# Performance work log

Measured on AMD Instinct MI355X. Metric: run time of the kernel, lower is better.

Reference implementation:

```python
import jax, jax.numpy as jnp
import numpy as np

B, C, N, H = 16, 256, 2048, 128


def setup_inputs() -> dict:
    key = jax.random.key(0)
    ks = jax.random.split(key, 9)
    s_in = 1.0 / np.sqrt(C)
    s_h = 1.0 / np.sqrt(H)
    return {
        "x": jax.random.normal(ks[0], (B, C, N), dtype=jnp.float32),
        "Wq": jax.random.uniform(ks[1], (H, C), jnp.float32, -s_in, s_in),
        "bq": jax.random.uniform(ks[2], (H,), jnp.float32, -s_in, s_in),
        "Wk": jax.random.uniform(ks[3], (H, C), jnp.float32, -s_in, s_in),
        "bk": jax.random.uniform(ks[4], (H,), jnp.float32, -s_in, s_in),
        "Wv": jax.random.uniform(ks[5], (H, C), jnp.float32, -s_in, s_in),
        "bv": jax.random.uniform(ks[6], (H,), jnp.float32, -s_in, s_in),
        "Wf": jax.random.uniform(ks[7], (C, H), jnp.float32, -s_h, s_h),
        "bf": jax.random.uniform(ks[8], (C,), jnp.float32, -s_h, s_h),
    }


def reference(x, Wq, bq, Wk, bk, Wv, bv, Wf, bf):
    # 1x1 conv == channel-wise linear: [B,C,N] -> [B,H,N]
    Q = jnp.einsum("bcn,hc->bhn", x, Wq) + bq[:, None]
    K = jnp.einsum("bcn,hc->bhn", x, Wk) + bk[:, None]
    V = jnp.einsum("bcn,hc->bhn", x, Wv) + bv[:, None]
    # attn[b, i, j] = softmax_j( Q[b,:,i] . K[b,:,j] )   (no sqrt(d) scaling, as in source)
    scores = jnp.einsum("bhi,bhj->bij", Q, K)          # [B, N, N]
    attn = jax.nn.softmax(scores, axis=-1)
    # out[b, h, i] = sum_j V[b,h,j] * attn[b,i,j]
    out = jnp.einsum("bhj,bij->bhi", V, attn)           # [B, H, N]
    out = jnp.einsum("bhn,ch->bcn", out, Wf) + bf[:, None]
    return out + x
```

## Files before the change

### kernel.cpp

```cpp
#include <hip/hip_runtime.h>
#include <hip/hip_bf16.h>

#define BATCH 16
#define CDIM 256
#define NDIM 2048
#define HDIM 128
#define KVB 128
#define NT (NDIM / KVB)

typedef __bf16 bf16;
typedef float f32x4 __attribute__((ext_vector_type(4)));
typedef float f32x16 __attribute__((ext_vector_type(16)));
typedef bf16 bf16x8 __attribute__((ext_vector_type(8)));
typedef unsigned int u32x4 __attribute__((ext_vector_type(4)));

#define LOG2E 1.4426950408889634f

__device__ __forceinline__ int swz512(int row, int colbyte) {
  return row * 512 + (colbyte ^ ((row & 15) << 4));
}
__device__ __forceinline__ int swz256(int row, int colbyte) {
  return row * 256 + (colbyte ^ ((row & 7) << 4));
}

__device__ __forceinline__ f32x4 mfma16(bf16x8 a, bf16x8 b, f32x4 c) {
  return __builtin_amdgcn_mfma_f32_16x16x32_bf16(a, b, c, 0, 0, 0);
}
__device__ __forceinline__ f32x16 mfma32(bf16x8 a, bf16x8 b, f32x16 c) {
  return __builtin_amdgcn_mfma_f32_32x32x16_bf16(a, b, c, 0, 0, 0);
}

__device__ __forceinline__ unsigned cvtpk(float lo, float hi) {
  unsigned r;
  asm("v_cvt_pk_bf16_f32 %0, %1, %2" : "=v"(r) : "v"(lo), "v"(hi));
  return r;
}
__device__ __forceinline__ void pswap(unsigned &a, unsigned &b) {
  asm volatile("v_permlane32_swap_b32 %0, %1" : "+v"(a), "+v"(b));
}

__device__ __forceinline__ void gload16(const bf16* g, char* l) {
  __builtin_amdgcn_global_load_lds(
      (const __attribute__((address_space(1))) void*)g,
      (__attribute__((address_space(3))) void*)l, 16, 0, 0);
}

__device__ __forceinline__ bf16x8 cvt8(float4 a, float4 b) {
  bf16x8 o;
  o[0] = (bf16)a.x; o[1] = (bf16)a.y; o[2] = (bf16)a.z; o[3] = (bf16)a.w;
  o[4] = (bf16)b.x; o[5] = (bf16)b.y; o[6] = (bf16)b.z; o[7] = (bf16)b.w;
  return o;
}

__global__ __launch_bounds__(256) void k1_qkv(
    const float* __restrict__ x,
    const float* __restrict__ Wq, const float* __restrict__ bq,
    const float* __restrict__ Wk, const float* __restrict__ bk,
    const float* __restrict__ Wv, const float* __restrict__ bv,
    bf16* __restrict__ Qo, bf16* __restrict__ Ko, bf16* __restrict__ Vo) {
  __shared__ char lds[65536];
  char* xT = lds;
  char* Wt = lds + 32768;

  const int t = threadIdx.x;
  const int l = t & 63;
  const int w = t >> 6;
  const int b = blockIdx.x >> 5;
  const int n0 = (blockIdx.x & 31) * 64;

#pragma unroll
  for (int pass = 0; pass < 16; ++pass) {
    int c = pass * 16 + (t >> 4);
    int nq = t & 15;
    const float4 v = *reinterpret_cast<const float4*>(
        x + (size_t)(b * CDIM + c) * NDIM + n0 + nq * 4);
    float fv[4] = {v.x, v.y, v.z, v.w};
#pragma unroll
    for (int i = 0; i < 4; ++i) {
      int row = nq * 4 + i;
      *reinterpret_cast<bf16*>(xT + swz512(row, c * 2)) = (bf16)fv[i];
    }
  }

  const float* Wp[3] = {Wq, Wk, Wv};
  const float* bp[3] = {bq, bk, bv};

#pragma unroll 1
  for (int p = 0; p < 3; ++p) {
    f32x4 acc[8];
#pragma unroll
    for (int i = 0; i < 8; ++i) acc[i] = f32x4{0.f, 0.f, 0.f, 0.f};

#pragma unroll 1
    for (int kh = 0; kh < 2; ++kh) {
      __syncthreads();
#pragma unroll
      for (int pass = 0; pass < 8; ++pass) {
        int h = pass * 16 + (t >> 4);
        int cq = t & 15;
        const float* src = Wp[p] + (size_t)h * CDIM + kh * 128 + cq * 8;
        float4 v0 = *reinterpret_cast<const float4*>(src);
        float4 v1 = *reinterpret_cast<const float4*>(src + 4);
        *reinterpret_cast<bf16x8*>(Wt + swz256(h, cq * 16)) = cvt8(v0, v1);
      }
      __syncthreads();

      if (p < 2) {
#pragma unroll
        for (int ks = 0; ks < 4; ++ks) {
          int cb2 = ks * 64 + (l >> 4) * 16;
          bf16x8 a = *reinterpret_cast<const bf16x8*>(
              xT + swz512(w * 16 + (l & 15), kh * 256 + cb2));
#pragma unroll
          for (int nf = 0; nf < 8; ++nf) {
            bf16x8 bb = *reinterpret_cast<const bf16x8*>(
                Wt + swz256(nf * 16 + (l & 15), cb2));
            acc[nf] = mfma16(a, bb, acc[nf]);
          }
        }
      } else {
#pragma unroll
        for (int ks = 0; ks < 4; ++ks) {
          int cb2 = ks * 64 + (l >> 4) * 16;
          bf16x8 a0 = *reinterpret_cast<const bf16x8*>(
              Wt + swz256(w * 32 + (l & 15), cb2));
          bf16x8 a1 = *reinterpret_cast<const bf16x8*>(
              Wt + swz256(w * 32 + 16 + (l & 15), cb2));
#pragma unroll
          for (int nf = 0; nf < 4; ++nf) {
            bf16x8 bb = *reinterpret_cast<const bf16x8*>(
                xT + swz512(nf * 16 + (l & 15), kh * 256 + cb2));
            acc[nf] = mfma16(a0, bb, acc[nf]);
            acc[4 + nf] = mfma16(a1, bb, acc[4 + nf]);
          }
        }
      }
    }

    if (p < 2) {
      bf16* dst = (p == 0) ? Qo : Ko;
#pragma unroll
      for (int nf = 0; nf < 8; ++nf) {
        float bias = bp[p][nf * 16 + (l & 15)];
#pragma unroll
        for (int r = 0; r < 4; ++r) {
          int n = n0 + w * 16 + (l >> 4) * 4 + r;
          int h = nf * 16 + (l & 15);
          dst[(size_t)(b * NDIM + n) * HDIM + h] = (bf16)(acc[nf][r] + bias);
        }
      }
    } else {
#pragma unroll
      for (int mf = 0; mf < 2; ++mf)
#pragma unroll
        for (int nf = 0; nf < 4; ++nf)
#pragma unroll
          for (int r = 0; r < 4; ++r) {
            int h = w * 32 + mf * 16 + (l >> 4) * 4 + r;
            int n = n0 + nf * 16 + (l & 15);
            Vo[(size_t)(b * HDIM + h) * NDIM + n] =
                (bf16)(acc[mf * 4 + nf][r] + bp[2][h]);
          }
    }
  }
}

__global__ __launch_bounds__(512, 2) void k2_attn(
    const bf16* __restrict__ Q, const bf16* __restrict__ K,
    const bf16* __restrict__ V, bf16* __restrict__ O) {
  extern __shared__ char lds[];

  const int t = threadIdx.x;
  const int l = t & 63;
  const int w = t >> 6;
  const int wm = w >> 1;
  const int wk = w & 1;
  const int hi = l >> 5;
  const int c31 = l & 31;

  const int pid = blockIdx.x;
  const int b = (pid & 7) * 2 + ((pid >> 3) >> 4);
  const int q0 = ((pid >> 3) & 15) * 128;

  bf16x8 qf[8];
  {
    const bf16* qrow = Q + (size_t)(b * NDIM + q0 + wm * 32 + c31) * HDIM + hi * 8;
#pragma unroll
    for (int cs = 0; cs < 8; ++cs)
      qf[cs] = *reinterpret_cast<const bf16x8*>(qrow + cs * 16);
  }

  const bool isV = (w >= 4);
  const int wv = isV ? (w - 4) : w;
  const int slot = l & 15;
  const bf16* gbase[8];
#pragma unroll
  for (int i = 0; i < 8; ++i) {
    int r = wv * 32 + (l >> 4) + i * 4;
    int so = (slot ^ (r & 15)) * 8;
    gbase[i] = isV ? (V + (size_t)(b * HDIM + r) * NDIM + so)
                   : (K + (size_t)(b * NDIM + r) * HDIM + so);
  }
  const size_t gstep = isV ? (size_t)KVB : (size_t)KVB * HDIM;
  const int stagebase = (isV ? 32768 : 0) + wv * 8192;

  f32x16 oacc[4];
#pragma unroll
  for (int dg = 0; dg < 4; ++dg)
#pragma unroll
    for (int r = 0; r < 16; ++r) oacc[dg][r] = 0.f;
  float m_run = -1.0e30f, l_run = 0.f;

#pragma unroll
  for (int i = 0; i < 8; ++i)
    gload16(gbase[i], lds + stagebase + i * 1024);

#pragma unroll 1
  for (int kt = 0; kt < NT; ++kt) {
    char* buf = lds + (kt & 1) * 65536;
    if (kt + 1 < NT) {
      char* nbuf = lds + ((kt + 1) & 1) * 65536;
      const size_t off = (size_t)(kt + 1) * gstep;
#pragma unroll
      for (int i = 0; i < 8; ++i)
        gload16(gbase[i] + off, nbuf + stagebase + i * 1024);
      asm volatile("s_waitcnt vmcnt(8)" ::: "memory");
    } else {
      asm volatile("s_waitcnt vmcnt(0)" ::: "memory");
    }
    __builtin_amdgcn_s_barrier();

    const char* Kt = buf;
    const char* Vt = buf + 32768;
    const int rx = l & 15;

    f32x16 s[2];
#pragma unroll
    for (int kg = 0; kg < 2; ++kg)
#pragma unroll
      for (int r = 0; r < 16; ++r) s[kg][r] = 0.f;
    __builtin_amdgcn_s_setprio(1);
#pragma unroll
    for (int kg = 0; kg < 2; ++kg) {
      const char* kr = Kt + (wk * 64 + kg * 32 + c31) * 256;
#pragma unroll
      for (int cs = 0; cs < 8; ++cs) {
        bf16x8 kf = *reinterpret_cast<const bf16x8*>(kr + (((cs * 2 + hi) ^ rx) * 16));
        s[kg] = mfma32(kf, qf[cs], s[kg]);
      }
    }
    __builtin_amdgcn_s_setprio(0);

    float mt = s[0][0];
#pragma unroll
    for (int r = 1; r < 16; ++r) mt = fmaxf(mt, s[0][r]);
#pragma unroll
    for (int r = 0; r < 16; ++r) mt = fmaxf(mt, s[1][r]);
    mt = fmaxf(mt, __shfl_xor(mt, 32));

    float fac = 1.0f;
    if (!__all(mt - m_run <= 8.0f)) {
      float mnew = fmaxf(m_run, mt);
      fac = __builtin_amdgcn_exp2f((m_run - mnew) * LOG2E);
      m_run = mnew;
      int fbits = __builtin_bit_cast(int, fac);
#pragma unroll
      for (int r = 0; r < 16; ++r) {
        int srcl = ((r & 3) + 8 * (r >> 2) + 4 * hi) * 4;
        float fr = __builtin_bit_cast(
            float, __builtin_amdgcn_ds_bpermute(srcl, fbits));
#pragma unroll
        for (int dg = 0; dg < 4; ++dg) oacc[dg][r] *= fr;
      }
    }

    float sum = 0.f;
#pragma unroll
    for (int kg = 0; kg < 2; ++kg)
#pragma unroll
      for (int r = 0; r < 16; ++r) {
        float p = __builtin_amdgcn_exp2f((s[kg][r] - m_run) * LOG2E);
        s[kg][r] = p;
        sum += p;
      }
    sum += __shfl_xor(sum, 32);
    l_run = l_run * fac + sum;

    __builtin_amdgcn_s_setprio(1);
#pragma unroll
    for (int kg = 0; kg < 2; ++kg) {
      unsigned w0 = cvtpk(s[kg][0], s[kg][1]);
      unsigned w1 = cvtpk(s[kg][2], s[kg][3]);
      unsigned w2 = cvtpk(s[kg][4], s[kg][5]);
      unsigned w3 = cvtpk(s[kg][6], s[kg][7]);
      unsigned w4 = cvtpk(s[kg][8], s[kg][9]);
      unsigned w5 = cvtpk(s[kg][10], s[kg][11]);
      unsigned w6 = cvtpk(s[kg][12], s[kg][13]);
      unsigned w7 = cvtpk(s[kg][14], s[kg][15]);
      pswap(w0, w2); pswap(w1, w3); pswap(w4, w6); pswap(w5, w7);
      u32x4 pw0 = {w0, w1, w2, w3};
      u32x4 pw1 = {w4, w5, w6, w7};
      bf16x8 pa0 = __builtin_bit_cast(bf16x8, pw0);
      bf16x8 pa1 = __builtin_bit_cast(bf16x8, pw1);
#pragma unroll
      for (int dg = 0; dg < 4; ++dg) {
        const char* vr = Vt + (dg * 32 + c31) * 256;
        bf16x8 vf0 = *reinterpret_cast<const bf16x8*>(
            vr + (((wk * 8 + kg * 4 + 0 + hi) ^ rx) * 16));
        oacc[dg] = mfma32(pa0, vf0, oacc[dg]);
        bf16x8 vf1 = *reinterpret_cast<const bf16x8*>(
            vr + (((wk * 8 + kg * 4 + 2 + hi) ^ rx) * 16));
        oacc[dg] = mfma32(pa1, vf1, oacc[dg]);
      }
    }
    __builtin_amdgcn_s_setprio(0);
    __builtin_amdgcn_s_barrier();
  }

  float* O1 = (float*)lds;
  float* M1 = (float*)(lds + 65536);
  float* L1 = (float*)(lds + 66560);
  float* G0 = (float*)(lds + 67584);
  float* G1 = (float*)(lds + 68608);

  if (wk == 1) {
#pragma unroll
    for (int dg = 0; dg < 4; ++dg)
#pragma unroll
      for (int r = 0; r < 16; ++r)
        O1[(((wm * 4 + dg) * 16 + r) << 6) + l] = oacc[dg][r];
    M1[wm * 64 + l] = m_run;
    L1[wm * 64 + l] = l_run;
  }
  __syncthreads();
  if (wk == 0) {
    float m1 = M1[wm * 64 + l];
    float l1v = L1[wm * 64 + l];
    float mf = fmaxf(m_run, m1);
    float a0 = __builtin_amdgcn_exp2f((m_run - mf) * LOG2E);
    float a1 = __builtin_amdgcn_exp2f((m1 - mf) * LOG2E);
    float lf = l_run * a0 + l1v * a1;
    G0[wm * 64 + l] = a0 / lf;
    G1[wm * 64 + l] = a1 / lf;
    asm volatile("s_waitcnt lgkmcnt(0)" ::: "memory");
    f32x4 g0v[4], g1v[4];
#pragma unroll
    for (int gi = 0; gi < 4; ++gi) {
      int qi = wm * 64 + hi * 32 + gi * 8 + hi * 4;
      g0v[gi] = *reinterpret_cast<const f32x4*>(&G0[qi]);
      g1v[gi] = *reinterpret_cast<const f32x4*>(&G1[qi]);
    }
#pragma unroll
    for (int dg = 0; dg < 4; ++dg) {
      int h = dg * 32 + c31;
#pragma unroll
      for (int r = 0; r < 16; ++r) {
        float o1 = O1[(((wm * 4 + dg) * 16 + r) << 6) + l];
        float val = oacc[dg][r] * g0v[r >> 2][r & 3] + o1 * g1v[r >> 2][r & 3];
        int n = q0 + wm * 32 + (r & 3) + 8 * (r >> 2) + 4 * hi;
        O[(size_t)(b * NDIM + n) * HDIM + h] = (bf16)val;
      }
    }
  }
}

__global__ __launch_bounds__(256) void k3_proj(
    const bf16* __restrict__ O, const float* __restrict__ Wf,
    const float* __restrict__ bfv, const float* __restrict__ x,
    float* __restrict__ out) {
  __shared__ char lds[49152];
  char* Wt = lds;
  char* Ot = lds + 32768;

  const int t = threadIdx.x;
  const int l = t & 63;
  const int w = t >> 6;
  const int b = blockIdx.x >> 5;
  const int n0 = (blockIdx.x & 31) * 64;

#pragma unroll
  for (int pass = 0; pass < 4; ++pass) {
    int n = pass * 16 + (t >> 4);
    int hq = t & 15;
    uint4 d = *reinterpret_cast<const uint4*>(
        O + (size_t)(b * NDIM + n0 + n) * HDIM + hq * 8);
    *reinterpret_cast<uint4*>(Ot + swz256(n, hq * 16)) = d;
  }

#pragma unroll 1
  for (int ch = 0; ch < 2; ++ch) {
    __syncthreads();
#pragma unroll
    for (int pass = 0; pass < 8; ++pass) {
      int cl = pass * 16 + (t >> 4);
      int hq = t & 15;
      const float* src = Wf + (size_t)(ch * 128 + cl) * HDIM + hq * 8;
      float4 v0 = *reinterpret_cast<const float4*>(src);
      float4 v1 = *reinterpret_cast<const float4*>(src + 4);
      *reinterpret_cast<bf16x8*>(Wt + swz256(cl, hq * 16)) = cvt8(v0, v1);
    }
    __syncthreads();

    f32x4 acc[2][4];
#pragma unroll
    for (int i = 0; i < 2; ++i)
#pragma unroll
      for (int j = 0; j < 4; ++j) acc[i][j] = f32x4{0.f, 0.f, 0.f, 0.f};

#pragma unroll
    for (int ks = 0; ks < 4; ++ks) {
      int cb = ks * 64 + (l >> 4) * 16;
      bf16x8 a0 = *reinterpret_cast<const bf16x8*>(
          Wt + swz256(w * 32 + (l & 15), cb));
      bf16x8 a1 = *reinterpret_cast<const bf16x8*>(
          Wt + swz256(w * 32 + 16 + (l & 15), cb));
#pragma unroll
      for (int nf = 0; nf < 4; ++nf) {
        bf16x8 bb = *reinterpret_cast<const bf16x8*>(
            Ot + swz256(nf * 16 + (l & 15), cb));
        acc[0][nf] = mfma16(a0, bb, acc[0][nf]);
        acc[1][nf] = mfma16(a1, bb, acc[1][nf]);
      }
    }

#pragma unroll
    for (int mf = 0; mf < 2; ++mf)
#pragma unroll
      for (int nf = 0; nf < 4; ++nf)
#pragma unroll
        for (int r = 0; r < 4; ++r) {
          int c = ch * 128 + w * 32 + mf * 16 + (l >> 4) * 4 + r;
          int n = n0 + nf * 16 + (l & 15);
          size_t idx = (size_t)(b * CDIM + c) * NDIM + n;
          out[idx] = acc[mf][nf][r] + bfv[c] + x[idx];
        }
  }
}

extern "C" void kernel_launch(void* const* d_in, const int* in_sizes, int n_in,
                              void* d_out, int out_size, void* d_ws,
                              size_t ws_size, hipStream_t stream) {
  (void)in_sizes; (void)n_in; (void)out_size;
  const float* x = (const float*)d_in[0];
  const float* Wq = (const float*)d_in[1];
  const float* bq = (const float*)d_in[2];
  const float* Wk = (const float*)d_in[3];
  const float* bk = (const float*)d_in[4];
  const float* Wv = (const float*)d_in[5];
  const float* bv = (const float*)d_in[6];
  const float* Wf = (const float*)d_in[7];
  const float* bfv = (const float*)d_in[8];
  float* out = (float*)d_out;

  if (ws_size < (24u << 20)) return;
  char* ws = (char*)d_ws;
  bf16* Qb = (bf16*)(ws);
  bf16* Kb = (bf16*)(ws + (8u << 20));
  bf16* Vb = (bf16*)(ws + (16u << 20));

  const unsigned k2_lds = 131072;
  hipFuncSetAttribute(reinterpret_cast<const void*>(k2_attn),
                      hipFuncAttributeMaxDynamicSharedMemorySize, (int)k2_lds);

  k1_qkv<<<512, 256, 0, stream>>>(x, Wq, bq, Wk, bk, Wv, bv, Qb, Kb, Vb);
  k2_attn<<<256, 512, k2_lds, stream>>>(Qb, Kb, Vb, Qb);
  k3_proj<<<512, 256, 0, stream>>>(Qb, Wf, bfv, x, out);
}
```

Before: 94.99 us.

## Repartition attention waves: each wave handles two query tiles over a quarter KV split

Wave work is reassigned so each of 8 waves covers 64 query rows (two 32-row subtiles) across a quarter of each KV tile, instead of 32 queries across half the tile. Every K and V fragment read from LDS now feeds two MFMAs, which halves LDS fragment traffic per MFMA. The cost is a four-way split-softmax merge through LDS with a tree reduction and extra barriers, plus doubled accumulator registers, which could hurt occupancy at 2 blocks per CU. Global load offsets also become 32-bit incremented integers rather than 64-bit pointers.

Result: slower. 119.6 us (+25.9%).

```diff
diff --git a/kernel.cpp b/kernel.cpp
--- a/kernel.cpp
+++ b/kernel.cpp
@@ -173,8 +173,8 @@
   const int t = threadIdx.x;
   const int l = t & 63;
   const int w = t >> 6;
-  const int wm = w >> 1;
-  const int wk = w & 1;
+  const int wm = w & 1;
+  const int wk = w >> 1;
   const int hi = l >> 5;
   const int c31 = l & 31;
 
@@ -182,48 +182,61 @@
   const int b = (pid & 7) * 2 + ((pid >> 3) >> 4);
   const int q0 = ((pid >> 3) & 15) * 128;
 
-  bf16x8 qf[8];
+  bf16x8 qf0[8], qf1[8];
   {
-    const bf16* qrow = Q + (size_t)(b * NDIM + q0 + wm * 32 + c31) * HDIM + hi * 8;
-#pragma unroll
-    for (int cs = 0; cs < 8; ++cs)
-      qf[cs] = *reinterpret_cast<const bf16x8*>(qrow + cs * 16);
+    const bf16* qb = Q + ((size_t)b * NDIM + q0 + wm * 64 + c31) * HDIM + hi * 8;
+#pragma unroll
+    for (int cs = 0; cs < 8; ++cs) {
+      qf0[cs] = *reinterpret_cast<const bf16x8*>(qb + cs * 16);
+      qf1[cs] = *reinterpret_cast<const bf16x8*>(qb + 32 * HDIM + cs * 16);
+    }
   }
 
   const bool isV = (w >= 4);
-  const int wv = isV ? (w - 4) : w;
+  const int wv = w & 3;
   const int slot = l & 15;
-  const bf16* gbase[8];
+  const bf16* gb = isV ? V : K;
+  unsigned off[8];
 #pragma unroll
   for (int i = 0; i < 8; ++i) {
     int r = wv * 32 + (l >> 4) + i * 4;
     int so = (slot ^ (r & 15)) * 8;
-    gbase[i] = isV ? (V + (size_t)(b * HDIM + r) * NDIM + so)
-                   : (K + (size_t)(b * NDIM + r) * HDIM + so);
-  }
-  const size_t gstep = isV ? (size_t)KVB : (size_t)KVB * HDIM;
+    off[i] = isV ? (unsigned)((b * HDIM + r) * NDIM + so)
+                 : (unsigned)((b * NDIM + r) * HDIM + so);
+  }
+  const unsigned gstep = isV ? (unsigned)KVB : (unsigned)(KVB * HDIM);
   const int stagebase = (isV ? 32768 : 0) + wv * 8192;
 
-  f32x16 oacc[4];
-#pragma unroll
-  for (int dg = 0; dg < 4; ++dg)
-#pragma unroll
-    for (int r = 0; r < 16; ++r) oacc[dg][r] = 0.f;
-  float m_run = -1.0e30f, l_run = 0.f;
+  f32x16 oacc[2][4];
+#pragma unroll
+  for (int qs = 0; qs < 2; ++qs)
+#pragma unroll
+    for (int dg = 0; dg < 4; ++dg)
+#pragma unroll
+      for (int r = 0; r < 16; ++r) oacc[qs][dg][r] = 0.f;
+  float m_run[2] = {-1.0e30f, -1.0e30f};
+  float l_run[2] = {0.f, 0.f};
 
 #pragma unroll
   for (int i = 0; i < 8; ++i)
-    gload16(gbase[i], lds + stagebase + i * 1024);
+    gload16(gb + off[i], lds + stagebase + i * 1024);
+
+  const int rx = l & 15;
+  const int kroff = (wk * 32 + c31) * 256;
+  const int vroff = c31 * 256;
+
+  bf16x8 pa[2][2];
 
 #pragma unroll 1
   for (int kt = 0; kt < NT; ++kt) {
     char* buf = lds + (kt & 1) * 65536;
     if (kt + 1 < NT) {
       char* nbuf = lds + ((kt + 1) & 1) * 65536;
-      const size_t off = (size_t)(kt + 1) * gstep;
-#pragma unroll
-      for (int i = 0; i < 8; ++i)
-        gload16(gbase[i] + off, nbuf + stagebase + i * 1024);
+#pragma unroll
+      for (int i = 0; i < 8; ++i) {
+        off[i] += gstep;
+        gload16(gb + off[i], nbuf + stagebase + i * 1024);
+      }
       asm volatile("s_waitcnt vmcnt(8)" ::: "memory");
     } else {
       asm volatile("s_waitcnt vmcnt(0)" ::: "memory");
@@ -232,135 +245,169 @@
 
     const char* Kt = buf;
     const char* Vt = buf + 32768;
-    const int rx = l & 15;
-
-    f32x16 s[2];
-#pragma unroll
-    for (int kg = 0; kg < 2; ++kg)
-#pragma unroll
-      for (int r = 0; r < 16; ++r) s[kg][r] = 0.f;
+
+    f32x16 s0, s1;
+#pragma unroll
+    for (int r = 0; r < 16; ++r) { s0[r] = 0.f; s1[r] = 0.f; }
     __builtin_amdgcn_s_setprio(1);
 #pragma unroll
-    for (int kg = 0; kg < 2; ++kg) {
-      const char* kr = Kt + (wk * 64 + kg * 32 + c31) * 256;
-#pragma unroll
-      for (int cs = 0; cs < 8; ++cs) {
-        bf16x8 kf = *reinterpret_cast<const bf16x8*>(kr + (((cs * 2 + hi) ^ rx) * 16));
-        s[kg] = mfma32(kf, qf[cs], s[kg]);
-      }
+    for (int cs = 0; cs < 8; ++cs) {
+      bf16x8 kf = *reinterpret_cast<const bf16x8*>(
+          Kt + kroff + (((cs * 2 + hi) ^ rx) * 16));
+      s0 = mfma32(kf, qf0[cs], s0);
+      s1 = mfma32(kf, qf1[cs], s1);
     }
     __builtin_amdgcn_s_setprio(0);
 
-    float mt = s[0][0];
-#pragma unroll
-    for (int r = 1; r < 16; ++r) mt = fmaxf(mt, s[0][r]);
-#pragma unroll
-    for (int r = 0; r < 16; ++r) mt = fmaxf(mt, s[1][r]);
-    mt = fmaxf(mt, __shfl_xor(mt, 32));
-
-    float fac = 1.0f;
-    if (!__all(mt - m_run <= 8.0f)) {
-      float mnew = fmaxf(m_run, mt);
-      fac = __builtin_amdgcn_exp2f((m_run - mnew) * LOG2E);
-      m_run = mnew;
-      int fbits = __builtin_bit_cast(int, fac);
+#pragma unroll
+    for (int qs = 0; qs < 2; ++qs) {
+      f32x16& s = qs ? s1 : s0;
+      float mt = s[0];
+#pragma unroll
+      for (int r = 1; r < 16; ++r) mt = fmaxf(mt, s[r]);
+      mt = fmaxf(mt, __shfl_xor(mt, 32));
+
+      float fac = 1.0f;
+      if (!__all(mt - m_run[qs] <= 8.0f)) {
+        float mnew = fmaxf(m_run[qs], mt);
+        fac = __builtin_amdgcn_exp2f((m_run[qs] - mnew) * LOG2E);
+        m_run[qs] = mnew;
+        int fbits = __builtin_bit_cast(int, fac);
+#pragma unroll
+        for (int r = 0; r < 16; ++r) {
+          int srcl = ((r & 3) + 8 * (r >> 2) + 4 * hi) * 4;
+          float fr = __builtin_bit_cast(
+              float, __builtin_amdgcn_ds_bpermute(srcl, fbits));
+#pragma unroll
+          for (int dg = 0; dg < 4; ++dg) oacc[qs][dg][r] *= fr;
+        }
+      }
+
+      float sum = 0.f;
 #pragma unroll
       for (int r = 0; r < 16; ++r) {
-        int srcl = ((r & 3) + 8 * (r >> 2) + 4 * hi) * 4;
-        float fr = __builtin_bit_cast(
-            float, __builtin_amdgcn_ds_bpermute(srcl, fbits));
-#pragma unroll
-        for (int dg = 0; dg < 4; ++dg) oacc[dg][r] *= fr;
-      }
-    }
-
-    float sum = 0.f;
-#pragma unroll
-    for (int kg = 0; kg < 2; ++kg)
-#pragma unroll
-      for (int r = 0; r < 16; ++r) {
-        float p = __builtin_amdgcn_exp2f((s[kg][r] - m_run) * LOG2E);
-        s[kg][r] = p;
+        float p = __builtin_amdgcn_exp2f((s[r] - m_run[qs]) * LOG2E);
+        s[r] = p;
         sum += p;
       }
-    sum += __shfl_xor(sum, 32);
-    l_run = l_run * fac + sum;
-
-    __builtin_amdgcn_s_setprio(1);
-#pragma unroll
-    for (int kg = 0; kg < 2; ++kg) {
-      unsigned w0 = cvtpk(s[kg][0], s[kg][1]);
-      unsigned w1 = cvtpk(s[kg][2], s[kg][3]);
-      unsigned w2 = cvtpk(s[kg][4], s[kg][5]);
-      unsigned w3 = cvtpk(s[kg][6], s[kg][7]);
-      unsigned w4 = cvtpk(s[kg][8], s[kg][9]);
-      unsigned w5 = cvtpk(s[kg][10], s[kg][11]);
-      unsigned w6 = cvtpk(s[kg][12], s[kg][13]);
-      unsigned w7 = cvtpk(s[kg][14], s[kg][15]);
+      sum += __shfl_xor(sum, 32);
+      l_run[qs] = l_run[qs] * fac + sum;
+
+      unsigned w0 = cvtpk(s[0], s[1]);
+      unsigned w1 = cvtpk(s[2], s[3]);
+      unsigned w2 = cvtpk(s[4], s[5]);
+      unsigned w3 = cvtpk(s[6], s[7]);
+      unsigned w4 = cvtpk(s[8], s[9]);
+      unsigned w5 = cvtpk(s[10], s[11]);
+      unsigned w6 = cvtpk(s[12], s[13]);
+      unsigned w7 = cvtpk(s[14], s[15]);
       pswap(w0, w2); pswap(w1, w3); pswap(w4, w6); pswap(w5, w7);
       u32x4 pw0 = {w0, w1, w2, w3};
       u32x4 pw1 = {w4, w5, w6, w7};
-      bf16x8 pa0 = __builtin_bit_cast(bf16x8, pw0);
-      bf16x8 pa1 = __builtin_bit_cast(bf16x8, pw1);
+      pa[qs][0] = __builtin_bit_cast(bf16x8, pw0);
+      pa[qs][1] = __builtin_bit_cast(bf16x8, pw1);
+    }
+
+    __builtin_amdgcn_s_setprio(1);
+#pragma unroll
+    for (int ks = 0; ks < 2; ++ks) {
 #pragma unroll
       for (int dg = 0; dg < 4; ++dg) {
-        const char* vr = Vt + (dg * 32 + c31) * 256;
-        bf16x8 vf0 = *reinterpret_cast<const bf16x8*>(
-            vr + (((wk * 8 + kg * 4 + 0 + hi) ^ rx) * 16));
-        oacc[dg] = mfma32(pa0, vf0, oacc[dg]);
-        bf16x8 vf1 = *reinterpret_cast<const bf16x8*>(
-            vr + (((wk * 8 + kg * 4 + 2 + hi) ^ rx) * 16));
-        oacc[dg] = mfma32(pa1, vf1, oacc[dg]);
+        bf16x8 vf = *reinterpret_cast<const bf16x8*>(
+            Vt + vroff + dg * 8192 + (((wk * 4 + ks * 2 + hi) ^ rx) * 16));
+        oacc[0][dg] = mfma32(pa[0][ks], vf, oacc[0][dg]);
+        oacc[1][dg] = mfma32(pa[1][ks], vf, oacc[1][dg]);
       }
     }
     __builtin_amdgcn_s_setprio(0);
     __builtin_amdgcn_s_barrier();
   }
 
-  float* O1 = (float*)lds;
-  float* M1 = (float*)(lds + 65536);
-  float* L1 = (float*)(lds + 66560);
-  float* G0 = (float*)(lds + 67584);
-  float* G1 = (float*)(lds + 68608);
-
-  if (wk == 1) {
-#pragma unroll
-    for (int dg = 0; dg < 4; ++dg)
-#pragma unroll
-      for (int r = 0; r < 16; ++r)
-        O1[(((wm * 4 + dg) * 16 + r) << 6) + l] = oacc[dg][r];
-    M1[wm * 64 + l] = m_run;
-    L1[wm * 64 + l] = l_run;
+  float* Ms = (float*)lds;
+  float* Ls = (float*)(lds + 2048);
+  if (l < 32) {
+#pragma unroll
+    for (int qs = 0; qs < 2; ++qs) {
+      int idx = ((wm * 2 + qs) * 4 + wk) * 32 + c31;
+      Ms[idx] = m_run[qs];
+      Ls[idx] = l_run[qs];
+    }
+  }
+  __syncthreads();
+  float scale[2];
+#pragma unroll
+  for (int qs = 0; qs < 2; ++qs) {
+    int base = (wm * 2 + qs) * 4 * 32 + c31;
+    float m0 = Ms[base], m1 = Ms[base + 32], m2 = Ms[base + 64], m3 = Ms[base + 96];
+    float mf = fmaxf(fmaxf(m0, m1), fmaxf(m2, m3));
+    float lf = __builtin_amdgcn_exp2f((m0 - mf) * LOG2E) * Ls[base] +
+               __builtin_amdgcn_exp2f((m1 - mf) * LOG2E) * Ls[base + 32] +
+               __builtin_amdgcn_exp2f((m2 - mf) * LOG2E) * Ls[base + 64] +
+               __builtin_amdgcn_exp2f((m3 - mf) * LOG2E) * Ls[base + 96];
+    scale[qs] = __builtin_amdgcn_exp2f((m_run[qs] - mf) * LOG2E) / lf;
+  }
+  __syncthreads();
+
+#pragma unroll
+  for (int qs = 0; qs < 2; ++qs) {
+    int sbits = __builtin_bit_cast(int, scale[qs]);
+#pragma unroll
+    for (int r = 0; r < 16; ++r) {
+      int srcl = ((r & 3) + 8 * (r >> 2) + 4 * hi) * 4;
+      float fr = __builtin_bit_cast(
+          float, __builtin_amdgcn_ds_bpermute(srcl, sbits));
+#pragma unroll
+      for (int dg = 0; dg < 4; ++dg) oacc[qs][dg][r] *= fr;
+    }
+  }
+
+  auto region = [&](int idx) { return (float*)(lds + idx * 32768); };
+  if (wk & 1) {
+    float* R = region(wm * 2 + (wk >> 1));
+#pragma unroll
+    for (int qs = 0; qs < 2; ++qs)
+#pragma unroll
+      for (int dg = 0; dg < 4; ++dg)
+#pragma unroll
+        for (int r = 0; r < 16; ++r)
+          R[((qs * 4 + dg) * 16 + r) * 64 + l] = oacc[qs][dg][r];
+  }
+  __syncthreads();
+  if (!(wk & 1)) {
+    float* R = region(wm * 2 + (wk >> 1));
+#pragma unroll
+    for (int qs = 0; qs < 2; ++qs)
+#pragma unroll
+      for (int dg = 0; dg < 4; ++dg)
+#pragma unroll
+        for (int r = 0; r < 16; ++r)
+          oacc[qs][dg][r] += R[((qs * 4 + dg) * 16 + r) * 64 + l];
+  }
+  __syncthreads();
+  if (wk == 2) {
+    float* R = region(wm);
+#pragma unroll
+    for (int qs = 0; qs < 2; ++qs)
+#pragma unroll
+      for (int dg = 0; dg < 4; ++dg)
+#pragma unroll
+        for (int r = 0; r < 16; ++r)
+          R[((qs * 4 + dg) * 16 + r) * 64 + l] = oacc[qs][dg][r];
   }
   __syncthreads();
   if (wk == 0) {
-    float m1 = M1[wm * 64 + l];
-    float l1v = L1[wm * 64 + l];
-    float mf = fmaxf(m_run, m1);
-    float a0 = __builtin_amdgcn_exp2f((m_run - mf) * LOG2E);
-    float a1 = __builtin_amdgcn_exp2f((m1 - mf) * LOG2E);
-    float lf = l_run * a0 + l1v * a1;
-    G0[wm * 64 + l] = a0 / lf;
-    G1[wm * 64 + l] = a1 / lf;
-    asm volatile("s_waitcnt lgkmcnt(0)" ::: "memory");
-    f32x4 g0v[4], g1v[4];
-#pragma unroll
-    for (int gi = 0; gi < 4; ++gi) {
-      int qi = wm * 64 + hi * 32 + gi * 8 + hi * 4;
-      g0v[gi] = *reinterpret_cast<const f32x4*>(&G0[qi]);
-      g1v[gi] = *reinterpret_cast<const f32x4*>(&G1[qi]);
-    }
-#pragma unroll
-    for (int dg = 0; dg < 4; ++dg) {
-      int h = dg * 32 + c31;
-#pragma unroll
-      for (int r = 0; r < 16; ++r) {
-        float o1 = O1[(((wm * 4 + dg) * 16 + r) << 6) + l];
-        float val = oacc[dg][r] * g0v[r >> 2][r & 3] + o1 * g1v[r >> 2][r & 3];
-        int n = q0 + wm * 32 + (r & 3) + 8 * (r >> 2) + 4 * hi;
-        O[(size_t)(b * NDIM + n) * HDIM + h] = (bf16)val;
-      }
-    }
+    float* R = region(wm);
+#pragma unroll
+    for (int qs = 0; qs < 2; ++qs)
+#pragma unroll
+      for (int dg = 0; dg < 4; ++dg)
+#pragma unroll
+        for (int r = 0; r < 16; ++r) {
+          float val = oacc[qs][dg][r] + R[((qs * 4 + dg) * 16 + r) * 64 + l];
+          int n = q0 + wm * 64 + qs * 32 + (r & 3) + 8 * (r >> 2) + 4 * hi;
+          int h = dg * 32 + c31;
+          O[((size_t)b * NDIM + n) * HDIM + h] = (bf16)val;
+        }
   }
 }
 
```
